# Kernel tuning notes

Measured on AMD Instinct MI355X. Metric: run time of the kernel, lower is better.

Reference implementation:

```python
import jax, jax.numpy as jnp
import numpy as np

B, T, I, H = 512, 512, 32, 64


def setup_inputs() -> dict:
    key = jax.random.key(0)
    ks = jax.random.split(key, 11)
    s_i = 1.0 / np.sqrt(H)  # PyTorch GRU init scale
    inp = {
        "x": jax.random.normal(ks[0], (B, T, I), dtype=jnp.float32),
        # layer 0 (input size I), layer 1 (input size H); gate order r,z,n
        "W_ih0": jax.random.uniform(ks[1], (3 * H, I), jnp.float32, -s_i, s_i),
        "W_hh0": jax.random.uniform(ks[2], (3 * H, H), jnp.float32, -s_i, s_i),
        "b_ih0": jax.random.uniform(ks[3], (3 * H,), jnp.float32, -s_i, s_i),
        "b_hh0": jax.random.uniform(ks[4], (3 * H,), jnp.float32, -s_i, s_i),
        "W_ih1": jax.random.uniform(ks[5], (3 * H, H), jnp.float32, -s_i, s_i),
        "W_hh1": jax.random.uniform(ks[6], (3 * H, H), jnp.float32, -s_i, s_i),
        "b_ih1": jax.random.uniform(ks[7], (3 * H,), jnp.float32, -s_i, s_i),
        "b_hh1": jax.random.uniform(ks[8], (3 * H,), jnp.float32, -s_i, s_i),
        "fc_w": jax.random.uniform(ks[9], (1, H), jnp.float32, -s_i, s_i),
        "fc_b": jax.random.uniform(ks[10], (1,), jnp.float32, -s_i, s_i),
    }
    return inp


def gru_layer(x, W_ih, W_hh, b_ih, b_hh):
    """One GRU layer over [B,T,D] -> [B,T,H]. PyTorch gate order r,z,n."""
    h = x.shape[-1] * 0  # placeholder, real H from W_hh
    H_ = W_hh.shape[1]
    # precompute input projections for all timesteps: [B,T,3H]
    gi = jnp.einsum("btd,gd->btg", x, W_ih) + b_ih
    gi = jnp.swapaxes(gi, 0, 1)  # [T,B,3H] for scan

    def step(h_prev, gi_t):
        gh = h_prev @ W_hh.T + b_hh  # [B,3H]
        i_r, i_z, i_n = jnp.split(gi_t, 3, axis=-1)
        h_r, h_z, h_n = jnp.split(gh, 3, axis=-1)
        r = jax.nn.sigmoid(i_r + h_r)
        z = jax.nn.sigmoid(i_z + h_z)
        n = jnp.tanh(i_n + r * h_n)
        h_new = (1.0 - z) * n + z * h_prev
        return h_new, h_new

    h0 = jnp.zeros((x.shape[0], H_), dtype=x.dtype)
    _, ys = jax.lax.scan(step, h0, gi)
    return jnp.swapaxes(ys, 0, 1)  # [B,T,H]


def reference(x, W_ih0, W_hh0, b_ih0, b_hh0, W_ih1, W_hh1, b_ih1, b_hh1, fc_w, fc_b):
    # dropout between layers is inactive in eval mode -> identity
    h1 = gru_layer(x, W_ih0, W_hh0, b_ih0, b_hh0)
    h2 = gru_layer(h1, W_ih1, W_hh1, b_ih1, b_hh1)
    last = h2[:, -1, :]  # [B,H]
    return last @ fc_w.T + fc_b  # [B,1]
```

## Files before the change

kernel.cpp:

```cpp
#include <hip/hip_runtime.h>

typedef _Float16 h2 __attribute__((ext_vector_type(2)));
typedef _Float16 h4 __attribute__((ext_vector_type(4)));
typedef _Float16 h8 __attribute__((ext_vector_type(8)));
typedef float    f4 __attribute__((ext_vector_type(4)));

#define TT 512
#define NB 512
#define II 32
#define HH 64
#define BT 16
#define LROW 72

static __device__ __forceinline__ float fexp2f(float x){ return __builtin_amdgcn_exp2f(x); }
static __device__ __forceinline__ float frcpf(float x){ return __builtin_amdgcn_rcpf(x); }
static __device__ __forceinline__ float sigf(float x){ return frcpf(1.0f + fexp2f(-1.442695040888963f*x)); }
static __device__ __forceinline__ float tanhf_fast(float x){ return 1.0f - 2.0f*frcpf(1.0f + fexp2f(2.885390081777926f*x)); }

struct H8S { h2 a,b,c,d; };
struct H4S { h2 a,b; };
static __device__ __forceinline__ h2 pkrtz(float a, float b){
  return __builtin_bit_cast(h2, __builtin_amdgcn_cvt_pkrtz(a, b));
}
static __device__ __forceinline__ h8 pack8(h2 a, h2 b, h2 c, h2 d){
  H8S s{a,b,c,d}; return __builtin_bit_cast(h8, s);
}
static __device__ __forceinline__ h8 cvt8(float4 a, float4 b){
  return pack8(pkrtz(a.x,a.y), pkrtz(a.z,a.w), pkrtz(b.x,b.y), pkrtz(b.z,b.w));
}
static __device__ __forceinline__ h8 ld8cvt(const float* p){
  return cvt8(((const float4*)p)[0], ((const float4*)p)[1]);
}
static __device__ __forceinline__ f4 mfma16(h8 a, h8 b, f4 c){
  return __builtin_amdgcn_mfma_f32_16x16x32_f16(a, b, c, 0, 0, 0);
}

static __device__ __forceinline__ void phase_barrier(){
  asm volatile("s_waitcnt lgkmcnt(0)" ::: "memory");
  __builtin_amdgcn_s_barrier();
  __builtin_amdgcn_sched_barrier(0);
  asm volatile("" ::: "memory");
}

__global__ __attribute__((amdgpu_flat_work_group_size(512,512)))
void gru2_pipe(
    const float* __restrict__ x,
    const float* __restrict__ Wih0, const float* __restrict__ Whh0,
    const float* __restrict__ bih0, const float* __restrict__ bhh0,
    const float* __restrict__ Wih1, const float* __restrict__ Whh1,
    const float* __restrict__ b_ih1, const float* __restrict__ b_hh1,
    const float* __restrict__ fcw, const float* __restrict__ fcb,
    float* __restrict__ out)
{
  const int tid  = threadIdx.x;
  const int w    = tid >> 6;
  const int lane = tid & 63;
  const int c    = lane & 15;
  const int g    = lane >> 4;
  const int wt   = w & 3;
  const bool isL0 = (w < 4);
  const int b0   = blockIdx.x * BT;

  __shared__ _Float16 h0L[2][16*LROW];
  __shared__ _Float16 h1L[2][16*LROW];
  __shared__ float    fcred[256];

  for (int i = tid; i < 16*LROW; i += 512){
    h0L[0][i] = (_Float16)0; h0L[1][i] = (_Float16)0;
    h1L[0][i] = (_Float16)0; h1L[1][i] = (_Float16)0;
  }

  const int r0 = 16*wt + c, r1 = 64 + 16*wt + c, r2 = 128 + 16*wt + c;
  const int j0 = 16*wt + 4*g;

  h8 Ax[3];
  h8 Ah[3][2];
  h8 P0[3][2];
  h8 P1[3][2];
  f4 brv, bzv, biv, bhv;

  if (isL0) {
    Ax[0] = ld8cvt(Wih0 + r0*II + 8*g);
    Ax[1] = ld8cvt(Wih0 + r1*II + 8*g);
    Ax[2] = ld8cvt(Wih0 + r2*II + 8*g);
#pragma unroll
    for (int q = 0; q < 2; ++q){
      Ah[0][q] = ld8cvt(Whh0 + r0*HH + 32*q + 8*g);
      Ah[1][q] = ld8cvt(Whh0 + r1*HH + 32*q + 8*g);
      Ah[2][q] = ld8cvt(Whh0 + r2*HH + 32*q + 8*g);
    }
#pragma unroll
    for (int i = 0; i < 4; ++i){
      brv[i] = bih0[j0+i]     + bhh0[j0+i];
      bzv[i] = bih0[64+j0+i]  + bhh0[64+j0+i];
      biv[i] = bih0[128+j0+i];
      bhv[i] = bhh0[128+j0+i];
    }
  } else {
#pragma unroll
    for (int q = 0; q < 2; ++q){
      P0[0][q] = ld8cvt(Wih1 + r0*HH + 32*q + 8*g);
      P0[1][q] = ld8cvt(Wih1 + r1*HH + 32*q + 8*g);
      P0[2][q] = ld8cvt(Wih1 + r2*HH + 32*q + 8*g);
      P1[0][q] = ld8cvt(Whh1 + r0*HH + 32*q + 8*g);
      P1[1][q] = ld8cvt(Whh1 + r1*HH + 32*q + 8*g);
      P1[2][q] = ld8cvt(Whh1 + r2*HH + 32*q + 8*g);
    }
#pragma unroll
    for (int i = 0; i < 4; ++i){
      brv[i] = b_ih1[j0+i]     + b_hh1[j0+i];
      bzv[i] = b_ih1[64+j0+i]  + b_hh1[64+j0+i];
      biv[i] = b_ih1[128+j0+i];
      bhv[i] = b_hh1[128+j0+i];
    }
  }

  float hp[4] = {0.f,0.f,0.f,0.f};

  const float* xrow = x + (size_t)(b0+c)*TT*II + 8*g;
  float4 x0a, x0b, x1a, x1b;
  if (isL0) {
    x0a = ((const float4*)xrow)[0];       x0b = ((const float4*)xrow)[1];
    x1a = ((const float4*)(xrow+II))[0];  x1b = ((const float4*)(xrow+II))[1];
  }

  int buf = 0;
  __syncthreads();

  for (int p = 0; p <= TT; ++p){
    if (isL0) {
      if (p < TT) {
        const _Float16* h0r = &h0L[buf][c*LROW];
        h8 ba = *(const h8*)(h0r + 8*g);
        h8 bb = *(const h8*)(h0r + 32 + 8*g);
        h8 bx = cvt8(x0a, x0b);
        f4 Cr = brv, Cz = bzv, Cni = biv, Cnh = bhv;
        Cr  = mfma16(Ax[0], bx, Cr);
        Cz  = mfma16(Ax[1], bx, Cz);
        Cni = mfma16(Ax[2], bx, Cni);
        Cr  = mfma16(Ah[0][0], ba, Cr);   Cr  = mfma16(Ah[0][1], bb, Cr);
        Cz  = mfma16(Ah[1][0], ba, Cz);   Cz  = mfma16(Ah[1][1], bb, Cz);
        Cnh = mfma16(Ah[2][0], ba, Cnh);  Cnh = mfma16(Ah[2][1], bb, Cnh);
        x0a = x1a; x0b = x1b;
        {
          const float* pn = xrow + (size_t)((p+2 < TT) ? (p+2) : (TT-1))*II;
          x1a = ((const float4*)pn)[0];  x1b = ((const float4*)pn)[1];
        }
#pragma unroll
        for (int i = 0; i < 4; ++i){
          const float r  = sigf(Cr[i]);
          const float z  = sigf(Cz[i]);
          const float nn = tanhf_fast(Cni[i] + r*Cnh[i]);
          hp[i] = nn + z*(hp[i] - nn);
        }
        H4S s{ pkrtz(hp[0], hp[1]), pkrtz(hp[2], hp[3]) };
        *(h4*)(&h0L[buf^1][c*LROW + j0]) = __builtin_bit_cast(h4, s);
      }
    } else {
      if (p >= 1) {
        const _Float16* h0r = &h0L[buf][c*LROW];
        const _Float16* h1r = &h1L[buf][c*LROW];
        h8 a0 = *(const h8*)(h0r + 8*g);
        h8 a1 = *(const h8*)(h0r + 32 + 8*g);
        h8 v0 = *(const h8*)(h1r + 8*g);
        h8 v1 = *(const h8*)(h1r + 32 + 8*g);
        f4 Dr = brv, Dz = bzv, Dni = biv, Dnh = bhv;
        Dr  = mfma16(P0[0][0], a0, Dr);   Dr  = mfma16(P0[0][1], a1, Dr);
        Dr  = mfma16(P1[0][0], v0, Dr);   Dr  = mfma16(P1[0][1], v1, Dr);
        Dz  = mfma16(P0[1][0], a0, Dz);   Dz  = mfma16(P0[1][1], a1, Dz);
        Dz  = mfma16(P1[1][0], v0, Dz);   Dz  = mfma16(P1[1][1], v1, Dz);
        Dni = mfma16(P0[2][0], a0, Dni);  Dni = mfma16(P0[2][1], a1, Dni);
        Dnh = mfma16(P1[2][0], v0, Dnh);  Dnh = mfma16(P1[2][1], v1, Dnh);
#pragma unroll
        for (int i = 0; i < 4; ++i){
          const float r  = sigf(Dr[i]);
          const float z  = sigf(Dz[i]);
          const float nn = tanhf_fast(Dni[i] + r*Dnh[i]);
          hp[i] = nn + z*(hp[i] - nn);
        }
        H4S s{ pkrtz(hp[0], hp[1]), pkrtz(hp[2], hp[3]) };
        *(h4*)(&h1L[buf^1][c*LROW + j0]) = __builtin_bit_cast(h4, s);
      }
    }
    phase_barrier();
    buf ^= 1;
  }

  if (!isL0) {
    float s = fcw[j0]*hp[0] + fcw[j0+1]*hp[1] + fcw[j0+2]*hp[2] + fcw[j0+3]*hp[3];
    fcred[(wt*4 + g)*16 + c] = s;
  }
  __syncthreads();
  if (tid < 16){
    float s = fcb[0];
#pragma unroll
    for (int q = 0; q < 16; ++q) s += fcred[q*16 + tid];
    out[b0 + tid] = s;
  }
}

extern "C" void kernel_launch(void* const* d_in, const int* in_sizes, int n_in,
                              void* d_out, int out_size, void* d_ws, size_t ws_size,
                              hipStream_t stream) {
  const float* x    = (const float*)d_in[0];
  const float* Wih0 = (const float*)d_in[1];
  const float* Whh0 = (const float*)d_in[2];
  const float* bih0 = (const float*)d_in[3];
  const float* bhh0 = (const float*)d_in[4];
  const float* Wih1 = (const float*)d_in[5];
  const float* Whh1 = (const float*)d_in[6];
  const float* bih1 = (const float*)d_in[7];
  const float* bhh1 = (const float*)d_in[8];
  const float* fcw  = (const float*)d_in[9];
  const float* fcb  = (const float*)d_in[10];
  float* out = (float*)d_out;

  gru2_pipe<<<dim3(NB/BT), dim3(512), 0, stream>>>(
      x, Wih0, Whh0, bih0, bhh0, Wih1, Whh1, bih1, bhh1, fcw, fcb, out);
}
```

Before: 306.6 us.

## Merge layer-0 and layer-1 waves so each wave runs both GRU layers

The block shrinks from 8 waves (4 for layer 0, 4 for layer 1) to 4 waves. Each wave now holds the weights for both layers and computes the layer-0 step for time p and the layer-1 step for time p-1 in the same phase, in a loop unrolled by two so the x prefetch registers alternate. This halves the number of waves meeting at every per-timestep barrier. It also gives the compiler two independent MFMA and activation chains to interleave within one wave. The sched_barrier after the barrier is dropped so instructions can be scheduled across it. The cost is a longer serial chain per wave and higher register pressure from holding both layers' weights.

```diff
diff --git a/kernel.cpp b/kernel.cpp
--- a/kernel.cpp
+++ b/kernel.cpp
@@ -38,12 +38,65 @@
 static __device__ __forceinline__ void phase_barrier(){
   asm volatile("s_waitcnt lgkmcnt(0)" ::: "memory");
   __builtin_amdgcn_s_barrier();
-  __builtin_amdgcn_sched_barrier(0);
   asm volatile("" ::: "memory");
 }
 
-__global__ __attribute__((amdgpu_flat_work_group_size(512,512)))
-void gru2_pipe(
+#define GPHASE(DOL0, DOL1, XA, XB, P)                                        \
+{                                                                            \
+  const _Float16* h0r = &h0L[buf][c*LROW];                                   \
+  h8 ba = *(const h8*)(h0r + 8*g);                                           \
+  h8 bb = *(const h8*)(h0r + 32 + 8*g);                                      \
+  f4 Dr, Dz, Dni, Dnh;                                                       \
+  if (DOL1) {                                                                \
+    const _Float16* h1r = &h1L[buf][c*LROW];                                 \
+    h8 v0 = *(const h8*)(h1r + 8*g);                                         \
+    h8 v1 = *(const h8*)(h1r + 32 + 8*g);                                    \
+    Dr = brv1; Dz = bzv1; Dni = biv1; Dnh = bhv1;                            \
+    Dr  = mfma16(P0[0][0], ba, Dr);   Dr  = mfma16(P0[0][1], bb, Dr);        \
+    Dr  = mfma16(P1[0][0], v0, Dr);   Dr  = mfma16(P1[0][1], v1, Dr);        \
+    Dz  = mfma16(P0[1][0], ba, Dz);   Dz  = mfma16(P0[1][1], bb, Dz);        \
+    Dz  = mfma16(P1[1][0], v0, Dz);   Dz  = mfma16(P1[1][1], v1, Dz);        \
+    Dni = mfma16(P0[2][0], ba, Dni);  Dni = mfma16(P0[2][1], bb, Dni);       \
+    Dnh = mfma16(P1[2][0], v0, Dnh);  Dnh = mfma16(P1[2][1], v1, Dnh);       \
+  }                                                                          \
+  if (DOL0) {                                                                \
+    h8 bx = cvt8(XA, XB);                                                    \
+    f4 Cr = brv0, Cz = bzv0, Cni = biv0, Cnh = bhv0;                         \
+    Cr  = mfma16(Ah[0][0], ba, Cr);   Cr  = mfma16(Ah[0][1], bb, Cr);        \
+    Cz  = mfma16(Ah[1][0], ba, Cz);   Cz  = mfma16(Ah[1][1], bb, Cz);        \
+    Cnh = mfma16(Ah[2][0], ba, Cnh);  Cnh = mfma16(Ah[2][1], bb, Cnh);       \
+    Cr  = mfma16(Ax[0], bx, Cr);                                             \
+    Cz  = mfma16(Ax[1], bx, Cz);                                             \
+    Cni = mfma16(Ax[2], bx, Cni);                                            \
+    { const float* pn = xrow + (size_t)(((P)+2 < TT) ? ((P)+2) : (TT-1))*II; \
+      XA = ((const float4*)pn)[0];  XB = ((const float4*)pn)[1]; }           \
+    _Pragma("unroll")                                                        \
+    for (int i = 0; i < 4; ++i){                                             \
+      const float r  = sigf(Cr[i]);                                          \
+      const float z  = sigf(Cz[i]);                                          \
+      const float nn = tanhf_fast(Cni[i] + r*Cnh[i]);                        \
+      hp0[i] = nn + z*(hp0[i] - nn);                                         \
+    }                                                                        \
+    H4S s0{ pkrtz(hp0[0], hp0[1]), pkrtz(hp0[2], hp0[3]) };                  \
+    *(h4*)(&h0L[buf^1][c*LROW + j0]) = __builtin_bit_cast(h4, s0);           \
+  }                                                                          \
+  if (DOL1) {                                                                \
+    _Pragma("unroll")                                                        \
+    for (int i = 0; i < 4; ++i){                                             \
+      const float r  = sigf(Dr[i]);                                          \
+      const float z  = sigf(Dz[i]);                                          \
+      const float nn = tanhf_fast(Dni[i] + r*Dnh[i]);                        \
+      hp1[i] = nn + z*(hp1[i] - nn);                                         \
+    }                                                                        \
+    H4S s1{ pkrtz(hp1[0], hp1[1]), pkrtz(hp1[2], hp1[3]) };                  \
+    *(h4*)(&h1L[buf^1][c*LROW + j0]) = __builtin_bit_cast(h4, s1);           \
+  }                                                                          \
+  phase_barrier();                                                           \
+  buf ^= 1;                                                                  \
+}
+
+__global__ __launch_bounds__(256, 1)
+void gru2_merged(
     const float* __restrict__ x,
     const float* __restrict__ Wih0, const float* __restrict__ Whh0,
     const float* __restrict__ bih0, const float* __restrict__ bhh0,
@@ -57,138 +110,75 @@
   const int lane = tid & 63;
   const int c    = lane & 15;
   const int g    = lane >> 4;
-  const int wt   = w & 3;
-  const bool isL0 = (w < 4);
   const int b0   = blockIdx.x * BT;
 
   __shared__ _Float16 h0L[2][16*LROW];
   __shared__ _Float16 h1L[2][16*LROW];
   __shared__ float    fcred[256];
 
-  for (int i = tid; i < 16*LROW; i += 512){
+  for (int i = tid; i < 16*LROW; i += 256){
     h0L[0][i] = (_Float16)0; h0L[1][i] = (_Float16)0;
     h1L[0][i] = (_Float16)0; h1L[1][i] = (_Float16)0;
   }
 
-  const int r0 = 16*wt + c, r1 = 64 + 16*wt + c, r2 = 128 + 16*wt + c;
-  const int j0 = 16*wt + 4*g;
+  const int r0 = 16*w + c, r1 = 64 + 16*w + c, r2 = 128 + 16*w + c;
+  const int j0 = 16*w + 4*g;
 
   h8 Ax[3];
   h8 Ah[3][2];
   h8 P0[3][2];
   h8 P1[3][2];
-  f4 brv, bzv, biv, bhv;
-
-  if (isL0) {
-    Ax[0] = ld8cvt(Wih0 + r0*II + 8*g);
-    Ax[1] = ld8cvt(Wih0 + r1*II + 8*g);
-    Ax[2] = ld8cvt(Wih0 + r2*II + 8*g);
+  Ax[0] = ld8cvt(Wih0 + r0*II + 8*g);
+  Ax[1] = ld8cvt(Wih0 + r1*II + 8*g);
+  Ax[2] = ld8cvt(Wih0 + r2*II + 8*g);
 #pragma unroll
-    for (int q = 0; q < 2; ++q){
-      Ah[0][q] = ld8cvt(Whh0 + r0*HH + 32*q + 8*g);
-      Ah[1][q] = ld8cvt(Whh0 + r1*HH + 32*q + 8*g);
-      Ah[2][q] = ld8cvt(Whh0 + r2*HH + 32*q + 8*g);
-    }
+  for (int q = 0; q < 2; ++q){
+    Ah[0][q] = ld8cvt(Whh0 + r0*HH + 32*q + 8*g);
+    Ah[1][q] = ld8cvt(Whh0 + r1*HH + 32*q + 8*g);
+    Ah[2][q] = ld8cvt(Whh0 + r2*HH + 32*q + 8*g);
+    P0[0][q] = ld8cvt(Wih1 + r0*HH + 32*q + 8*g);
+    P0[1][q] = ld8cvt(Wih1 + r1*HH + 32*q + 8*g);
+    P0[2][q] = ld8cvt(Wih1 + r2*HH + 32*q + 8*g);
+    P1[0][q] = ld8cvt(Whh1 + r0*HH + 32*q + 8*g);
+    P1[1][q] = ld8cvt(Whh1 + r1*HH + 32*q + 8*g);
+    P1[2][q] = ld8cvt(Whh1 + r2*HH + 32*q + 8*g);
+  }
+
+  f4 brv0, bzv0, biv0, bhv0, brv1, bzv1, biv1, bhv1;
 #pragma unroll
-    for (int i = 0; i < 4; ++i){
-      brv[i] = bih0[j0+i]     + bhh0[j0+i];
-      bzv[i] = bih0[64+j0+i]  + bhh0[64+j0+i];
-      biv[i] = bih0[128+j0+i];
-      bhv[i] = bhh0[128+j0+i];
-    }
-  } else {
-#pragma unroll
-    for (int q = 0; q < 2; ++q){
-      P0[0][q] = ld8cvt(Wih1 + r0*HH + 32*q + 8*g);
-      P0[1][q] = ld8cvt(Wih1 + r1*HH + 32*q + 8*g);
-      P0[2][q] = ld8cvt(Wih1 + r2*HH + 32*q + 8*g);
-      P1[0][q] = ld8cvt(Whh1 + r0*HH + 32*q + 8*g);
-      P1[1][q] = ld8cvt(Whh1 + r1*HH + 32*q + 8*g);
-      P1[2][q] = ld8cvt(Whh1 + r2*HH + 32*q + 8*g);
-    }
-#pragma unroll
-    for (int i = 0; i < 4; ++i){
-      brv[i] = b_ih1[j0+i]     + b_hh1[j0+i];
-      bzv[i] = b_ih1[64+j0+i]  + b_hh1[64+j0+i];
-      biv[i] = b_ih1[128+j0+i];
-      bhv[i] = b_hh1[128+j0+i];
-    }
-  }
-
-  float hp[4] = {0.f,0.f,0.f,0.f};
+  for (int i = 0; i < 4; ++i){
+    brv0[i] = bih0[j0+i]      + bhh0[j0+i];
+    bzv0[i] = bih0[64+j0+i]   + bhh0[64+j0+i];
+    biv0[i] = bih0[128+j0+i];
+    bhv0[i] = bhh0[128+j0+i];
+    brv1[i] = b_ih1[j0+i]     + b_hh1[j0+i];
+    bzv1[i] = b_ih1[64+j0+i]  + b_hh1[64+j0+i];
+    biv1[i] = b_ih1[128+j0+i];
+    bhv1[i] = b_hh1[128+j0+i];
+  }
+
+  float hp0[4] = {0.f,0.f,0.f,0.f};
+  float hp1[4] = {0.f,0.f,0.f,0.f};
 
   const float* xrow = x + (size_t)(b0+c)*TT*II + 8*g;
   float4 x0a, x0b, x1a, x1b;
-  if (isL0) {
-    x0a = ((const float4*)xrow)[0];       x0b = ((const float4*)xrow)[1];
-    x1a = ((const float4*)(xrow+II))[0];  x1b = ((const float4*)(xrow+II))[1];
-  }
+  x0a = ((const float4*)xrow)[0];       x0b = ((const float4*)xrow)[1];
+  x1a = ((const float4*)(xrow+II))[0];  x1b = ((const float4*)(xrow+II))[1];
 
   int buf = 0;
   __syncthreads();
 
-  for (int p = 0; p <= TT; ++p){
-    if (isL0) {
-      if (p < TT) {
-        const _Float16* h0r = &h0L[buf][c*LROW];
-        h8 ba = *(const h8*)(h0r + 8*g);
-        h8 bb = *(const h8*)(h0r + 32 + 8*g);
-        h8 bx = cvt8(x0a, x0b);
-        f4 Cr = brv, Cz = bzv, Cni = biv, Cnh = bhv;
-        Cr  = mfma16(Ax[0], bx, Cr);
-        Cz  = mfma16(Ax[1], bx, Cz);
-        Cni = mfma16(Ax[2], bx, Cni);
-        Cr  = mfma16(Ah[0][0], ba, Cr);   Cr  = mfma16(Ah[0][1], bb, Cr);
-        Cz  = mfma16(Ah[1][0], ba, Cz);   Cz  = mfma16(Ah[1][1], bb, Cz);
-        Cnh = mfma16(Ah[2][0], ba, Cnh);  Cnh = mfma16(Ah[2][1], bb, Cnh);
-        x0a = x1a; x0b = x1b;
-        {
-          const float* pn = xrow + (size_t)((p+2 < TT) ? (p+2) : (TT-1))*II;
-          x1a = ((const float4*)pn)[0];  x1b = ((const float4*)pn)[1];
-        }
-#pragma unroll
-        for (int i = 0; i < 4; ++i){
-          const float r  = sigf(Cr[i]);
-          const float z  = sigf(Cz[i]);
-          const float nn = tanhf_fast(Cni[i] + r*Cnh[i]);
-          hp[i] = nn + z*(hp[i] - nn);
-        }
-        H4S s{ pkrtz(hp[0], hp[1]), pkrtz(hp[2], hp[3]) };
-        *(h4*)(&h0L[buf^1][c*LROW + j0]) = __builtin_bit_cast(h4, s);
-      }
-    } else {
-      if (p >= 1) {
-        const _Float16* h0r = &h0L[buf][c*LROW];
-        const _Float16* h1r = &h1L[buf][c*LROW];
-        h8 a0 = *(const h8*)(h0r + 8*g);
-        h8 a1 = *(const h8*)(h0r + 32 + 8*g);
-        h8 v0 = *(const h8*)(h1r + 8*g);
-        h8 v1 = *(const h8*)(h1r + 32 + 8*g);
-        f4 Dr = brv, Dz = bzv, Dni = biv, Dnh = bhv;
-        Dr  = mfma16(P0[0][0], a0, Dr);   Dr  = mfma16(P0[0][1], a1, Dr);
-        Dr  = mfma16(P1[0][0], v0, Dr);   Dr  = mfma16(P1[0][1], v1, Dr);
-        Dz  = mfma16(P0[1][0], a0, Dz);   Dz  = mfma16(P0[1][1], a1, Dz);
-        Dz  = mfma16(P1[1][0], v0, Dz);   Dz  = mfma16(P1[1][1], v1, Dz);
-        Dni = mfma16(P0[2][0], a0, Dni);  Dni = mfma16(P0[2][1], a1, Dni);
-        Dnh = mfma16(P1[2][0], v0, Dnh);  Dnh = mfma16(P1[2][1], v1, Dnh);
-#pragma unroll
-        for (int i = 0; i < 4; ++i){
-          const float r  = sigf(Dr[i]);
-          const float z  = sigf(Dz[i]);
-          const float nn = tanhf_fast(Dni[i] + r*Dnh[i]);
-          hp[i] = nn + z*(hp[i] - nn);
-        }
-        H4S s{ pkrtz(hp[0], hp[1]), pkrtz(hp[2], hp[3]) };
-        *(h4*)(&h1L[buf^1][c*LROW + j0]) = __builtin_bit_cast(h4, s);
-      }
-    }
-    phase_barrier();
-    buf ^= 1;
-  }
-
-  if (!isL0) {
-    float s = fcw[j0]*hp[0] + fcw[j0+1]*hp[1] + fcw[j0+2]*hp[2] + fcw[j0+3]*hp[3];
-    fcred[(wt*4 + g)*16 + c] = s;
+  GPHASE(true, false, x0a, x0b, 0);
+  for (int p = 1; p < TT-1; p += 2){
+    GPHASE(true, true, x1a, x1b, p);
+    GPHASE(true, true, x0a, x0b, p+1);
+  }
+  GPHASE(true, true, x1a, x1b, TT-1);
+  GPHASE(false, true, x0a, x0b, 0);
+
+  {
+    float s = fcw[j0]*hp1[0] + fcw[j0+1]*hp1[1] + fcw[j0+2]*hp1[2] + fcw[j0+3]*hp1[3];
+    fcred[(w*4 + g)*16 + c] = s;
   }
   __syncthreads();
   if (tid < 16){
@@ -215,6 +205,6 @@
   const float* fcb  = (const float*)d_in[10];
   float* out = (float*)d_out;
 
-  gru2_pipe<<<dim3(NB/BT), dim3(512), 0, stream>>>(
+  gru2_merged<<<dim3(NB/BT), dim3(256), 0, stream>>>(
       x, Wih0, Whh0, bih0, bhh0, Wih1, Whh1, bih1, bhh1, fcw, fcb, out);
 }
```

Measured after the change: 313.1 us. 1.02x slower.
